# Kernel optimization log

Measured on AMD Instinct MI355X. Metric: run time of the kernel, lower is better.

## Reference

```python
import jax, jax.numpy as jnp
import numpy as np

D = 64  # hidden_dim


def _bn(x, gamma, beta):
    # eval-mode BatchNorm1d with running_mean=0, running_var=1 (fresh model)
    return gamma * x + beta


def _edge_conv(h, W, b, gamma, beta):
    # h: [B,N,D]; W: [2D,D] split into Wi (acts on x_i) and Wj (acts on x_j)
    Wi, Wj = W[:D], W[D:]
    ti = jnp.einsum('bnd,de->bne', h, Wi)  # [B,N,D] (i term)
    tj = jnp.einsum('bmd,de->bme', h, Wj)  # [B,N,D] (j term)
    # e[b,i,j,:] = x_i@Wi + x_j@Wj + b  -> relu -> BN -> max over j
    e = ti[:, :, None, :] + tj[:, None, :, :] + b  # [B,N,N,D]
    e = _bn(jax.nn.relu(e), gamma, beta)
    return e.max(axis=2)  # [B,N,D]


def setup_inputs() -> dict:
    key = jax.random.key(0)
    ks = jax.random.split(key, 16)
    s = lambda k, shp, sc: (jax.random.normal(k, shp, dtype=jnp.float32) * sc)
    inp = {
        'x': s(ks[0], (32, 256, 4), 1.0),
        'W1': s(ks[1], (4, D), 0.5), 'b1': s(ks[2], (D,), 0.1),
        'g1': 1.0 + s(ks[3], (D,), 0.1), 'beta1': s(ks[4], (D,), 0.1),
        'We1': s(ks[5], (2 * D, D), 0.1), 'be1': s(ks[6], (D,), 0.1),
        'ge1': 1.0 + s(ks[7], (D,), 0.1), 'betae1': s(ks[8], (D,), 0.1),
        'We2': s(ks[9], (2 * D, D), 0.1), 'be2': s(ks[10], (D,), 0.1),
        'ge2': 1.0 + s(ks[11], (D,), 0.1), 'betae2': s(ks[12], (D,), 0.1),
        'Wg1': s(ks[13], (2 * D, D), 0.1), 'bg1': s(ks[14], (D,), 0.1),
        'Wg2': s(ks[15], (D, 2), 0.1), 'bg2': jnp.zeros((2,), jnp.float32),
    }
    return inp


def reference(x, W1, b1, g1, beta1, We1, be1, ge1, betae1, We2, be2, ge2, betae2, Wg1, bg1, Wg2, bg2):
    # input MLP: Linear -> ReLU -> BN (eval)
    h = _bn(jax.nn.relu(x @ W1 + b1), g1, beta1)  # [B,N,D]
    h = _edge_conv(h, We1, be1, ge1, betae1)
    h = _edge_conv(h, We2, be2, ge2, betae2)
    x_mean = h.mean(axis=1)  # [B,D]
    x_max = h.max(axis=1)    # [B,D]
    xg = jnp.concatenate([x_mean, x_max], axis=-1)  # [B,2D]
    # global MLP (dropout is identity in eval)
    out = jax.nn.relu(xg @ Wg1 + bg1) @ Wg2 + bg2  # [B,2]
    return out
```

## Files before the change

kernel.cpp:

```cpp
#include <hip/hip_runtime.h>

#define NB 32
#define NN 256
#define DD 64
#define SROW 68
#define FMAXV 3.402823466e+38f


__global__ __launch_bounds__(1024, 4) void k_all(
    const float* __restrict__ x,
    const float* __restrict__ W1,  const float* __restrict__ b1,
    const float* __restrict__ g1,  const float* __restrict__ beta1,
    const float* __restrict__ We1, const float* __restrict__ be1,
    const float* __restrict__ ge1, const float* __restrict__ bte1,
    const float* __restrict__ We2, const float* __restrict__ be2,
    const float* __restrict__ ge2, const float* __restrict__ bte2,
    const float* __restrict__ Wg1, const float* __restrict__ bg1,
    const float* __restrict__ Wg2, const float* __restrict__ bg2,
    float* __restrict__ out)
{
    __shared__ __align__(16) float Hs[NN * SROW];
    __shared__ float xg[2 * DD];
    __shared__ float hid[DD];

    const int b  = blockIdx.x;
    const int l  = threadIdx.x & 63;
    const int w  = __builtin_amdgcn_readfirstlane(threadIdx.x >> 6);
    const int d0 = w * 4;

#pragma unroll
    for (int cc = 0; cc < 4; ++cc) {
        const int n = cc * 64 + l;
        float4 xv = *(const float4*)(x + ((size_t)b * NN + n) * 4);
        float a[4];
#pragma unroll
        for (int j = 0; j < 4; ++j) a[j] = b1[d0 + j];
#pragma unroll
        for (int j = 0; j < 4; ++j) a[j] = fmaf(xv.x, W1[0 * DD + d0 + j], a[j]);
#pragma unroll
        for (int j = 0; j < 4; ++j) a[j] = fmaf(xv.y, W1[1 * DD + d0 + j], a[j]);
#pragma unroll
        for (int j = 0; j < 4; ++j) a[j] = fmaf(xv.z, W1[2 * DD + d0 + j], a[j]);
#pragma unroll
        for (int j = 0; j < 4; ++j) a[j] = fmaf(xv.w, W1[3 * DD + d0 + j], a[j]);
        float h[4];
#pragma unroll
        for (int j = 0; j < 4; ++j) h[j] = g1[d0 + j] * fmaxf(a[j], 0.f) + beta1[d0 + j];
        *(float4*)(Hs + (size_t)n * SROW + d0) = make_float4(h[0], h[1], h[2], h[3]);
    }
    __syncthreads();

    float ti[4][4];
    float rmax[4], rmin[4];

    {
        float mx[4] = {-FMAXV, -FMAXV, -FMAXV, -FMAXV};
        float mn[4] = { FMAXV,  FMAXV,  FMAXV,  FMAXV};
#pragma unroll
        for (int cc = 0; cc < 4; ++cc) {
            float tj[4] = {0.f, 0.f, 0.f, 0.f};
#pragma unroll
            for (int j = 0; j < 4; ++j) ti[cc][j] = 0.f;
            const float* hrow = Hs + (size_t)(cc * 64 + l) * SROW;
#pragma unroll
            for (int k4 = 0; k4 < 16; ++k4) {
                float4 hv = *(const float4*)(hrow + k4 * 4);
                const float hk[4] = {hv.x, hv.y, hv.z, hv.w};
#pragma unroll
                for (int kk = 0; kk < 4; ++kk) {
                    const int k = k4 * 4 + kk;
                    const float* wi = We1 + k * DD + d0;
                    const float* wj = We1 + (DD + k) * DD + d0;
#pragma unroll
                    for (int j = 0; j < 4; ++j) {
                        ti[cc][j] = fmaf(hk[kk], wi[j], ti[cc][j]);
                        tj[j]     = fmaf(hk[kk], wj[j], tj[j]);
                    }
                }
            }
#pragma unroll
            for (int j = 0; j < 4; ++j) {
                mx[j] = fmaxf(mx[j], tj[j]);
                mn[j] = fminf(mn[j], tj[j]);
            }
        }
#pragma unroll
        for (int m = 1; m < 64; m <<= 1) {
#pragma unroll
            for (int j = 0; j < 4; ++j) {
                mx[j] = fmaxf(mx[j], __shfl_xor(mx[j], m, 64));
                mn[j] = fminf(mn[j], __shfl_xor(mn[j], m, 64));
            }
        }
#pragma unroll
        for (int j = 0; j < 4; ++j) { rmax[j] = mx[j]; rmin[j] = mn[j]; }
    }
    __syncthreads();

#pragma unroll
    for (int cc = 0; cc < 4; ++cc) {
        const int n = cc * 64 + l;
        float h[4];
#pragma unroll
        for (int j = 0; j < 4; ++j) {
            float gv = ge1[d0 + j];
            float sv = ti[cc][j] + (gv >= 0.f ? rmax[j] : rmin[j]) + be1[d0 + j];
            h[j] = gv * fmaxf(sv, 0.f) + bte1[d0 + j];
        }
        *(float4*)(Hs + (size_t)n * SROW + d0) = make_float4(h[0], h[1], h[2], h[3]);
    }
    __syncthreads();

    {
        float mx[4] = {-FMAXV, -FMAXV, -FMAXV, -FMAXV};
        float mn[4] = { FMAXV,  FMAXV,  FMAXV,  FMAXV};
#pragma unroll
        for (int cc = 0; cc < 4; ++cc) {
            float tj[4] = {0.f, 0.f, 0.f, 0.f};
#pragma unroll
            for (int j = 0; j < 4; ++j) ti[cc][j] = 0.f;
            const float* hrow = Hs + (size_t)(cc * 64 + l) * SROW;
#pragma unroll
            for (int k4 = 0; k4 < 16; ++k4) {
                float4 hv = *(const float4*)(hrow + k4 * 4);
                const float hk[4] = {hv.x, hv.y, hv.z, hv.w};
#pragma unroll
                for (int kk = 0; kk < 4; ++kk) {
                    const int k = k4 * 4 + kk;
                    const float* wi = We2 + k * DD + d0;
                    const float* wj = We2 + (DD + k) * DD + d0;
#pragma unroll
                    for (int j = 0; j < 4; ++j) {
                        ti[cc][j] = fmaf(hk[kk], wi[j], ti[cc][j]);
                        tj[j]     = fmaf(hk[kk], wj[j], tj[j]);
                    }
                }
            }
#pragma unroll
            for (int j = 0; j < 4; ++j) {
                mx[j] = fmaxf(mx[j], tj[j]);
                mn[j] = fminf(mn[j], tj[j]);
            }
        }
#pragma unroll
        for (int m = 1; m < 64; m <<= 1) {
#pragma unroll
            for (int j = 0; j < 4; ++j) {
                mx[j] = fmaxf(mx[j], __shfl_xor(mx[j], m, 64));
                mn[j] = fminf(mn[j], __shfl_xor(mn[j], m, 64));
            }
        }
#pragma unroll
        for (int j = 0; j < 4; ++j) { rmax[j] = mx[j]; rmin[j] = mn[j]; }
    }

    {
        float sm[4]  = {0.f, 0.f, 0.f, 0.f};
        float mxp[4] = {-FMAXV, -FMAXV, -FMAXV, -FMAXV};
#pragma unroll
        for (int cc = 0; cc < 4; ++cc) {
#pragma unroll
            for (int j = 0; j < 4; ++j) {
                float gv = ge2[d0 + j];
                float sv = ti[cc][j] + (gv >= 0.f ? rmax[j] : rmin[j]) + be2[d0 + j];
                float hv = gv * fmaxf(sv, 0.f) + bte2[d0 + j];
                sm[j]  += hv;
                mxp[j]  = fmaxf(mxp[j], hv);
            }
        }
#pragma unroll
        for (int m = 1; m < 64; m <<= 1) {
#pragma unroll
            for (int j = 0; j < 4; ++j) {
                sm[j]  += __shfl_xor(sm[j], m, 64);
                mxp[j]  = fmaxf(mxp[j], __shfl_xor(mxp[j], m, 64));
            }
        }
        float ssm = sm[0], smxp = mxp[0];
#pragma unroll
        for (int j = 1; j < 4; ++j) {
            ssm  = (l == j) ? sm[j]  : ssm;
            smxp = (l == j) ? mxp[j] : smxp;
        }
        if (l < 4) {
            xg[d0 + l]      = ssm * (1.f / 256.f);
            xg[DD + d0 + l] = smxp;
        }
    }
    __syncthreads();

    const int t = threadIdx.x;
    if (t < DD) {
        float a = bg1[t];
#pragma unroll
        for (int k = 0; k < 2 * DD; ++k) a = fmaf(xg[k], Wg1[k * DD + t], a);
        hid[t] = fmaxf(a, 0.f);
    }
    __syncthreads();
    if (t < 2) {
        float o = bg2[t];
#pragma unroll
        for (int j = 0; j < DD; ++j) o = fmaf(hid[j], Wg2[j * 2 + t], o);
        out[b * 2 + t] = o;
    }
}

extern "C" void kernel_launch(void* const* d_in, const int* in_sizes, int n_in,
                              void* d_out, int out_size, void* d_ws, size_t ws_size,
                              hipStream_t stream) {
    const float* x     = (const float*)d_in[0];
    const float* W1    = (const float*)d_in[1];
    const float* b1    = (const float*)d_in[2];
    const float* g1    = (const float*)d_in[3];
    const float* beta1 = (const float*)d_in[4];
    const float* We1   = (const float*)d_in[5];
    const float* be1   = (const float*)d_in[6];
    const float* ge1   = (const float*)d_in[7];
    const float* bte1  = (const float*)d_in[8];
    const float* We2   = (const float*)d_in[9];
    const float* be2   = (const float*)d_in[10];
    const float* ge2   = (const float*)d_in[11];
    const float* bte2  = (const float*)d_in[12];
    const float* Wg1   = (const float*)d_in[13];
    const float* bg1   = (const float*)d_in[14];
    const float* Wg2   = (const float*)d_in[15];
    const float* bg2   = (const float*)d_in[16];

    k_all<<<dim3(NB), dim3(1024), 0, stream>>>(
        x, W1, b1, g1, beta1,
        We1, be1, ge1, bte1,
        We2, be2, ge2, bte2,
        Wg1, bg1, Wg2, bg2, (float*)d_out);
}
```

Before: 130.8 us.

## Split fused kernel into three launches to spread work across more blocks

Replaces the single 32-block fused kernel with three kernels: two edge-conv kernels with 256 blocks each (split over node groups and half of the feature dims) and a tail kernel for pooling and the global MLP. The i-terms and partial per-group max/min of the j-terms pass through global workspace, and a later kernel reduces the four partials. This aims to fill far more compute units than 32 blocks can on the GPU. The cost is extra launches, global memory round trips, and recomputing the input MLP for all 64 dims in every thread of the first kernel.

New measurement: 122.1 us. -6.6%, faster.

```diff
diff --git a/kernel.cpp b/kernel.cpp
--- a/kernel.cpp
+++ b/kernel.cpp
@@ -7,185 +7,222 @@
 #define FMAXV 3.402823466e+38f
 
 
-__global__ __launch_bounds__(1024, 4) void k_all(
+__global__ __launch_bounds__(512, 2) void k1_conv(
     const float* __restrict__ x,
     const float* __restrict__ W1,  const float* __restrict__ b1,
     const float* __restrict__ g1,  const float* __restrict__ beta1,
-    const float* __restrict__ We1, const float* __restrict__ be1,
-    const float* __restrict__ ge1, const float* __restrict__ bte1,
-    const float* __restrict__ We2, const float* __restrict__ be2,
-    const float* __restrict__ ge2, const float* __restrict__ bte2,
+    const float* __restrict__ We1,
+    float* __restrict__ TI, float* __restrict__ PMAX, float* __restrict__ PMIN)
+{
+    const int blk = blockIdx.x;
+    const int b   = blk >> 3;
+    const int g   = (blk >> 1) & 3;
+    const int dh  = blk & 1;
+    const int l   = threadIdx.x & 63;
+    const int w   = __builtin_amdgcn_readfirstlane(threadIdx.x >> 6);
+    const int n   = g * 64 + l;
+    const int d0  = dh * 32 + w * 4;
+
+    float h[DD];
+    {
+        float4 xv = *(const float4*)(x + ((size_t)b * NN + n) * 4);
+#pragma unroll
+        for (int j = 0; j < DD; ++j) {
+            float a = b1[j];
+            a = fmaf(xv.x, W1[0 * DD + j], a);
+            a = fmaf(xv.y, W1[1 * DD + j], a);
+            a = fmaf(xv.z, W1[2 * DD + j], a);
+            a = fmaf(xv.w, W1[3 * DD + j], a);
+            h[j] = g1[j] * fmaxf(a, 0.f) + beta1[j];
+        }
+    }
+
+    float ti[4] = {0.f, 0.f, 0.f, 0.f}, tj[4] = {0.f, 0.f, 0.f, 0.f};
+#pragma unroll
+    for (int k = 0; k < DD; ++k) {
+        const float* wi = We1 + k * DD + d0;
+        const float* wj = We1 + (DD + k) * DD + d0;
+#pragma unroll
+        for (int j = 0; j < 4; ++j) {
+            ti[j] = fmaf(h[k], wi[j], ti[j]);
+            tj[j] = fmaf(h[k], wj[j], tj[j]);
+        }
+    }
+    *(float4*)(TI + ((size_t)(b * NN + n)) * DD + d0) =
+        make_float4(ti[0], ti[1], ti[2], ti[3]);
+
+    float mx[4], mn[4];
+#pragma unroll
+    for (int j = 0; j < 4; ++j) { mx[j] = tj[j]; mn[j] = tj[j]; }
+#pragma unroll
+    for (int m = 1; m < 64; m <<= 1) {
+#pragma unroll
+        for (int j = 0; j < 4; ++j) {
+            mx[j] = fmaxf(mx[j], __shfl_xor(mx[j], m, 64));
+            mn[j] = fminf(mn[j], __shfl_xor(mn[j], m, 64));
+        }
+    }
+    float smx = mx[0], smn = mn[0];
+#pragma unroll
+    for (int j = 1; j < 4; ++j) {
+        smx = (l == j) ? mx[j] : smx;
+        smn = (l == j) ? mn[j] : smn;
+    }
+    if (l < 4) {
+        PMAX[(b * 4 + g) * DD + d0 + l] = smx;
+        PMIN[(b * 4 + g) * DD + d0 + l] = smn;
+    }
+}
+
+__global__ __launch_bounds__(512, 2) void k2_conv(
+    const float* __restrict__ PMAXin, const float* __restrict__ PMINin,
+    const float* __restrict__ be1P, const float* __restrict__ ge1P,
+    const float* __restrict__ bte1P,
+    const float* __restrict__ We2,
+    const float* __restrict__ TIin,
+    float* __restrict__ TI2, float* __restrict__ PMAX, float* __restrict__ PMIN)
+{
+    __shared__ __align__(16) float Hs[64 * SROW];
+    const int blk = blockIdx.x;
+    const int b   = blk >> 3;
+    const int g   = (blk >> 1) & 3;
+    const int dh  = blk & 1;
+    const int l   = threadIdx.x & 63;
+    const int w   = __builtin_amdgcn_readfirstlane(threadIdx.x >> 6);
+    const int n   = g * 64 + l;
+    const int d0  = dh * 32 + w * 4;
+    const int s0  = w * 8;
+
+    {
+        float rmax[8], rmin[8];
+#pragma unroll
+        for (int j = 0; j < 8; ++j) {
+            const int base = b * 4 * DD + s0 + j;
+            rmax[j] = fmaxf(fmaxf(PMAXin[base],          PMAXin[base + DD]),
+                            fmaxf(PMAXin[base + 2 * DD], PMAXin[base + 3 * DD]));
+            rmin[j] = fminf(fminf(PMINin[base],          PMINin[base + DD]),
+                            fminf(PMINin[base + 2 * DD], PMINin[base + 3 * DD]));
+        }
+        const float* tip = TIin + ((size_t)(b * NN + n)) * DD + s0;
+        float4 t0 = *(const float4*)tip;
+        float4 t1 = *(const float4*)(tip + 4);
+        float tiv[8] = {t0.x, t0.y, t0.z, t0.w, t1.x, t1.y, t1.z, t1.w};
+        float hh[8];
+#pragma unroll
+        for (int j = 0; j < 8; ++j) {
+            float gv = ge1P[s0 + j];
+            float sv = tiv[j] + (gv >= 0.f ? rmax[j] : rmin[j]) + be1P[s0 + j];
+            hh[j] = gv * fmaxf(sv, 0.f) + bte1P[s0 + j];
+        }
+        *(float4*)(Hs + l * SROW + s0)     = make_float4(hh[0], hh[1], hh[2], hh[3]);
+        *(float4*)(Hs + l * SROW + s0 + 4) = make_float4(hh[4], hh[5], hh[6], hh[7]);
+    }
+    __syncthreads();
+
+    float h[DD];
+#pragma unroll
+    for (int q = 0; q < 16; ++q) {
+        float4 hv = *(const float4*)(Hs + l * SROW + q * 4);
+        h[q * 4 + 0] = hv.x; h[q * 4 + 1] = hv.y;
+        h[q * 4 + 2] = hv.z; h[q * 4 + 3] = hv.w;
+    }
+
+    float ti[4] = {0.f, 0.f, 0.f, 0.f}, tj[4] = {0.f, 0.f, 0.f, 0.f};
+#pragma unroll
+    for (int k = 0; k < DD; ++k) {
+        const float* wi = We2 + k * DD + d0;
+        const float* wj = We2 + (DD + k) * DD + d0;
+#pragma unroll
+        for (int j = 0; j < 4; ++j) {
+            ti[j] = fmaf(h[k], wi[j], ti[j]);
+            tj[j] = fmaf(h[k], wj[j], tj[j]);
+        }
+    }
+    *(float4*)(TI2 + ((size_t)(b * NN + n)) * DD + d0) =
+        make_float4(ti[0], ti[1], ti[2], ti[3]);
+
+    float mx[4], mn[4];
+#pragma unroll
+    for (int j = 0; j < 4; ++j) { mx[j] = tj[j]; mn[j] = tj[j]; }
+#pragma unroll
+    for (int m = 1; m < 64; m <<= 1) {
+#pragma unroll
+        for (int j = 0; j < 4; ++j) {
+            mx[j] = fmaxf(mx[j], __shfl_xor(mx[j], m, 64));
+            mn[j] = fminf(mn[j], __shfl_xor(mn[j], m, 64));
+        }
+    }
+    float smx = mx[0], smn = mn[0];
+#pragma unroll
+    for (int j = 1; j < 4; ++j) {
+        smx = (l == j) ? mx[j] : smx;
+        smn = (l == j) ? mn[j] : smn;
+    }
+    if (l < 4) {
+        PMAX[(b * 4 + g) * DD + d0 + l] = smx;
+        PMIN[(b * 4 + g) * DD + d0 + l] = smn;
+    }
+}
+
+__global__ __launch_bounds__(512) void k3_tail(
+    const float* __restrict__ PMAXin, const float* __restrict__ PMINin,
+    const float* __restrict__ be2P, const float* __restrict__ ge2P,
+    const float* __restrict__ bte2P,
+    const float* __restrict__ TI2,
     const float* __restrict__ Wg1, const float* __restrict__ bg1,
     const float* __restrict__ Wg2, const float* __restrict__ bg2,
     float* __restrict__ out)
 {
-    __shared__ __align__(16) float Hs[NN * SROW];
     __shared__ float xg[2 * DD];
     __shared__ float hid[DD];
-
     const int b  = blockIdx.x;
     const int l  = threadIdx.x & 63;
     const int w  = __builtin_amdgcn_readfirstlane(threadIdx.x >> 6);
-    const int d0 = w * 4;
-
+    const int d0 = w * 8;
+
+    float rmax[8], rmin[8];
+#pragma unroll
+    for (int j = 0; j < 8; ++j) {
+        const int base = b * 4 * DD + d0 + j;
+        rmax[j] = fmaxf(fmaxf(PMAXin[base],          PMAXin[base + DD]),
+                        fmaxf(PMAXin[base + 2 * DD], PMAXin[base + 3 * DD]));
+        rmin[j] = fminf(fminf(PMINin[base],          PMINin[base + DD]),
+                        fminf(PMINin[base + 2 * DD], PMINin[base + 3 * DD]));
+    }
+    float sm[8]  = {0.f, 0.f, 0.f, 0.f, 0.f, 0.f, 0.f, 0.f};
+    float mxp[8] = {-FMAXV, -FMAXV, -FMAXV, -FMAXV, -FMAXV, -FMAXV, -FMAXV, -FMAXV};
 #pragma unroll
     for (int cc = 0; cc < 4; ++cc) {
-        const int n = cc * 64 + l;
-        float4 xv = *(const float4*)(x + ((size_t)b * NN + n) * 4);
-        float a[4];
-#pragma unroll
-        for (int j = 0; j < 4; ++j) a[j] = b1[d0 + j];
-#pragma unroll
-        for (int j = 0; j < 4; ++j) a[j] = fmaf(xv.x, W1[0 * DD + d0 + j], a[j]);
-#pragma unroll
-        for (int j = 0; j < 4; ++j) a[j] = fmaf(xv.y, W1[1 * DD + d0 + j], a[j]);
-#pragma unroll
-        for (int j = 0; j < 4; ++j) a[j] = fmaf(xv.z, W1[2 * DD + d0 + j], a[j]);
-#pragma unroll
-        for (int j = 0; j < 4; ++j) a[j] = fmaf(xv.w, W1[3 * DD + d0 + j], a[j]);
-        float h[4];
-#pragma unroll
-        for (int j = 0; j < 4; ++j) h[j] = g1[d0 + j] * fmaxf(a[j], 0.f) + beta1[d0 + j];
-        *(float4*)(Hs + (size_t)n * SROW + d0) = make_float4(h[0], h[1], h[2], h[3]);
-    }
-    __syncthreads();
-
-    float ti[4][4];
-    float rmax[4], rmin[4];
-
-    {
-        float mx[4] = {-FMAXV, -FMAXV, -FMAXV, -FMAXV};
-        float mn[4] = { FMAXV,  FMAXV,  FMAXV,  FMAXV};
-#pragma unroll
-        for (int cc = 0; cc < 4; ++cc) {
-            float tj[4] = {0.f, 0.f, 0.f, 0.f};
-#pragma unroll
-            for (int j = 0; j < 4; ++j) ti[cc][j] = 0.f;
-            const float* hrow = Hs + (size_t)(cc * 64 + l) * SROW;
-#pragma unroll
-            for (int k4 = 0; k4 < 16; ++k4) {
-                float4 hv = *(const float4*)(hrow + k4 * 4);
-                const float hk[4] = {hv.x, hv.y, hv.z, hv.w};
-#pragma unroll
-                for (int kk = 0; kk < 4; ++kk) {
-                    const int k = k4 * 4 + kk;
-                    const float* wi = We1 + k * DD + d0;
-                    const float* wj = We1 + (DD + k) * DD + d0;
-#pragma unroll
-                    for (int j = 0; j < 4; ++j) {
-                        ti[cc][j] = fmaf(hk[kk], wi[j], ti[cc][j]);
-                        tj[j]     = fmaf(hk[kk], wj[j], tj[j]);
-                    }
-                }
-            }
-#pragma unroll
-            for (int j = 0; j < 4; ++j) {
-                mx[j] = fmaxf(mx[j], tj[j]);
-                mn[j] = fminf(mn[j], tj[j]);
-            }
-        }
-#pragma unroll
-        for (int m = 1; m < 64; m <<= 1) {
-#pragma unroll
-            for (int j = 0; j < 4; ++j) {
-                mx[j] = fmaxf(mx[j], __shfl_xor(mx[j], m, 64));
-                mn[j] = fminf(mn[j], __shfl_xor(mn[j], m, 64));
-            }
-        }
-#pragma unroll
-        for (int j = 0; j < 4; ++j) { rmax[j] = mx[j]; rmin[j] = mn[j]; }
-    }
-    __syncthreads();
-
-#pragma unroll
-    for (int cc = 0; cc < 4; ++cc) {
-        const int n = cc * 64 + l;
-        float h[4];
-#pragma unroll
-        for (int j = 0; j < 4; ++j) {
-            float gv = ge1[d0 + j];
-            float sv = ti[cc][j] + (gv >= 0.f ? rmax[j] : rmin[j]) + be1[d0 + j];
-            h[j] = gv * fmaxf(sv, 0.f) + bte1[d0 + j];
-        }
-        *(float4*)(Hs + (size_t)n * SROW + d0) = make_float4(h[0], h[1], h[2], h[3]);
-    }
-    __syncthreads();
-
-    {
-        float mx[4] = {-FMAXV, -FMAXV, -FMAXV, -FMAXV};
-        float mn[4] = { FMAXV,  FMAXV,  FMAXV,  FMAXV};
-#pragma unroll
-        for (int cc = 0; cc < 4; ++cc) {
-            float tj[4] = {0.f, 0.f, 0.f, 0.f};
-#pragma unroll
-            for (int j = 0; j < 4; ++j) ti[cc][j] = 0.f;
-            const float* hrow = Hs + (size_t)(cc * 64 + l) * SROW;
-#pragma unroll
-            for (int k4 = 0; k4 < 16; ++k4) {
-                float4 hv = *(const float4*)(hrow + k4 * 4);
-                const float hk[4] = {hv.x, hv.y, hv.z, hv.w};
-#pragma unroll
-                for (int kk = 0; kk < 4; ++kk) {
-                    const int k = k4 * 4 + kk;
-                    const float* wi = We2 + k * DD + d0;
-                    const float* wj = We2 + (DD + k) * DD + d0;
-#pragma unroll
-                    for (int j = 0; j < 4; ++j) {
-                        ti[cc][j] = fmaf(hk[kk], wi[j], ti[cc][j]);
-                        tj[j]     = fmaf(hk[kk], wj[j], tj[j]);
-                    }
-                }
-            }
-#pragma unroll
-            for (int j = 0; j < 4; ++j) {
-                mx[j] = fmaxf(mx[j], tj[j]);
-                mn[j] = fminf(mn[j], tj[j]);
-            }
-        }
-#pragma unroll
-        for (int m = 1; m < 64; m <<= 1) {
-#pragma unroll
-            for (int j = 0; j < 4; ++j) {
-                mx[j] = fmaxf(mx[j], __shfl_xor(mx[j], m, 64));
-                mn[j] = fminf(mn[j], __shfl_xor(mn[j], m, 64));
-            }
-        }
-#pragma unroll
-        for (int j = 0; j < 4; ++j) { rmax[j] = mx[j]; rmin[j] = mn[j]; }
-    }
-
-    {
-        float sm[4]  = {0.f, 0.f, 0.f, 0.f};
-        float mxp[4] = {-FMAXV, -FMAXV, -FMAXV, -FMAXV};
-#pragma unroll
-        for (int cc = 0; cc < 4; ++cc) {
-#pragma unroll
-            for (int j = 0; j < 4; ++j) {
-                float gv = ge2[d0 + j];
-                float sv = ti[cc][j] + (gv >= 0.f ? rmax[j] : rmin[j]) + be2[d0 + j];
-                float hv = gv * fmaxf(sv, 0.f) + bte2[d0 + j];
-                sm[j]  += hv;
-                mxp[j]  = fmaxf(mxp[j], hv);
-            }
-        }
-#pragma unroll
-        for (int m = 1; m < 64; m <<= 1) {
-#pragma unroll
-            for (int j = 0; j < 4; ++j) {
-                sm[j]  += __shfl_xor(sm[j], m, 64);
-                mxp[j]  = fmaxf(mxp[j], __shfl_xor(mxp[j], m, 64));
-            }
-        }
-        float ssm = sm[0], smxp = mxp[0];
-#pragma unroll
-        for (int j = 1; j < 4; ++j) {
-            ssm  = (l == j) ? sm[j]  : ssm;
-            smxp = (l == j) ? mxp[j] : smxp;
-        }
-        if (l < 4) {
-            xg[d0 + l]      = ssm * (1.f / 256.f);
-            xg[DD + d0 + l] = smxp;
-        }
+        const float* tip = TI2 + ((size_t)(b * NN + cc * 64 + l)) * DD + d0;
+        float4 t0 = *(const float4*)tip;
+        float4 t1 = *(const float4*)(tip + 4);
+        float tiv[8] = {t0.x, t0.y, t0.z, t0.w, t1.x, t1.y, t1.z, t1.w};
+#pragma unroll
+        for (int j = 0; j < 8; ++j) {
+            float gv = ge2P[d0 + j];
+            float sv = tiv[j] + (gv >= 0.f ? rmax[j] : rmin[j]) + be2P[d0 + j];
+            float hv = gv * fmaxf(sv, 0.f) + bte2P[d0 + j];
+            sm[j]  += hv;
+            mxp[j]  = fmaxf(mxp[j], hv);
+        }
+    }
+#pragma unroll
+    for (int m = 1; m < 64; m <<= 1) {
+#pragma unroll
+        for (int j = 0; j < 8; ++j) {
+            sm[j]  += __shfl_xor(sm[j], m, 64);
+            mxp[j]  = fmaxf(mxp[j], __shfl_xor(mxp[j], m, 64));
+        }
+    }
+    float ssm = sm[0], smxp = mxp[0];
+#pragma unroll
+    for (int j = 1; j < 8; ++j) {
+        ssm  = (l == j) ? sm[j]  : ssm;
+        smxp = (l == j) ? mxp[j] : smxp;
+    }
+    if (l < 8) {
+        xg[d0 + l]      = ssm * (1.f / 256.f);
+        xg[DD + d0 + l] = smxp;
     }
     __syncthreads();
 
@@ -226,9 +263,18 @@
     const float* Wg2   = (const float*)d_in[15];
     const float* bg2   = (const float*)d_in[16];
 
-    k_all<<<dim3(NB), dim3(1024), 0, stream>>>(
-        x, W1, b1, g1, beta1,
-        We1, be1, ge1, bte1,
-        We2, be2, ge2, bte2,
-        Wg1, bg1, Wg2, bg2, (float*)d_out);
-}
+    float* ws    = (float*)d_ws;
+    float* TI1   = ws;
+    float* TI2   = ws + 524288;
+    float* PMAX1 = ws + 1048576;
+    float* PMIN1 = ws + 1056768;
+    float* PMAX2 = ws + 1064960;
+    float* PMIN2 = ws + 1073152;
+
+    k1_conv<<<dim3(NB * 8), dim3(512), 0, stream>>>(
+        x, W1, b1, g1, beta1, We1, TI1, PMAX1, PMIN1);
+    k2_conv<<<dim3(NB * 8), dim3(512), 0, stream>>>(
+        PMAX1, PMIN1, be1, ge1, bte1, We2, TI1, TI2, PMAX2, PMIN2);
+    k3_tail<<<dim3(NB), dim3(512), 0, stream>>>(
+        PMAX2, PMIN2, be2, ge2, bte2, TI2, Wg1, bg1, Wg2, bg2, (float*)d_out);
+}
```
